# Kernel optimization log

Hardware: AMD Instinct MI355X
Metric: run time of the kernel (lower is better)

## Reference

```python
import jax, jax.numpy as jnp
import numpy as np

NUM_CLASSES = 10
THRESHOLD = 2e-4
ENT_COEF = 2e-4
COS_EPS = 1e-8
LOG_EPS = 1e-12


def setup_inputs() -> dict:
    key = jax.random.key(0)
    k1, k2, k3 = jax.random.split(key, 3)
    B, C, H, W = 256, 256, 8, 8
    M, F = 2000, C * H * W
    z = jax.random.normal(k1, (B, C, H, W), dtype=jnp.float32)
    labels = jax.random.randint(k2, (B,), 0, NUM_CLASSES)
    # kaiming-uniform-like init for the memory table
    bound = float(np.sqrt(6.0 / F))
    memory = jax.random.uniform(k3, (M, F), dtype=jnp.float32, minval=-bound, maxval=bound)
    return {"z": z, "labels": labels, "memory": memory}


def _shrink_l1norm(w):
    # hardshrink (strict |x| > lambda) then L1 renormalize along memories
    w = jnp.where(jnp.abs(w) > THRESHOLD, w, jnp.zeros_like(w))
    return w / jnp.sum(jnp.abs(w), axis=1, keepdims=True)


def _entropy_loss(w):
    return ENT_COEF * jnp.sum(-w * jnp.log(w + LOG_EPS))


def reference(z, labels, memory):
    B, C, H, W = z.shape
    M, F = memory.shape
    zf = z.reshape(B, F)
    # cosine similarity without materializing (B, M, F): dot / max(||z||*||m||, eps)
    nz = jnp.linalg.norm(zf, axis=1)              # (B,)
    nm = jnp.linalg.norm(memory, axis=1)          # (M,)
    logit = (zf @ memory.T) / jnp.maximum(nz[:, None] * nm[None, :], COS_EPS)  # (B, M)
    mem_weight = jax.nn.softmax(logit, axis=1)
    # per-class masks: memory slots are partitioned contiguously per class
    mem_per_class = M // NUM_CLASSES
    cls_of_mem = jnp.arange(M) // mem_per_class   # (M,)
    m1 = (cls_of_mem[None, :] == labels[:, None]).astype(mem_weight.dtype)  # target mask
    m2 = 1.0 - m1
    w_t = _shrink_l1norm(mem_weight * m1)
    w_nt = _shrink_l1norm(mem_weight * m2)
    z_hat_target = (w_t @ memory).reshape(B, C, H, W)
    z_hat_non_target = (w_nt @ memory).reshape(B, C, H, W)
    return (z_hat_target, z_hat_non_target, _entropy_loss(w_t), _entropy_loss(w_nt))
```

## Files before the change

### kernel.cpp

```cpp
#include <hip/hip_runtime.h>
#include <math.h>

#define BATCH 256
#define FDIM 16384
#define MSLOTS 2000
#define MPAD 2048
#define NCLS 10
#define MPC 200
#define NFB2 128

static constexpr float THRESH = 2e-4f;
static constexpr float ENTC   = 2e-4f;
static constexpr float CEPS   = 1e-8f;
static constexpr float LEPS   = 1e-12f;

using bf16x8 = __attribute__((ext_vector_type(8))) short;
using f32x4  = __attribute__((ext_vector_type(4))) float;
using us8    = __attribute__((ext_vector_type(8))) unsigned short;
using f4v    = __attribute__((ext_vector_type(4))) float;
using u4v    = __attribute__((ext_vector_type(4))) unsigned int;

__device__ __forceinline__ unsigned short f2bf(float f) {
  unsigned u = __float_as_uint(f);
  unsigned r = u + 0x7fffu + ((u >> 16) & 1u);
  return (unsigned short)(r >> 16);
}

__device__ __forceinline__ void gload_lds16(const unsigned short* g, unsigned short* l) {
  __builtin_amdgcn_global_load_lds(
      (const __attribute__((address_space(1))) void*)g,
      (__attribute__((address_space(3))) void*)l, 16, 0, 0);
}

__device__ __forceinline__ float waveReduceSum(float v) {
#pragma unroll
  for (int o = 32; o > 0; o >>= 1) v += __shfl_xor(v, o);
  return v;
}
__device__ __forceinline__ float waveReduceMax(float v) {
#pragma unroll
  for (int o = 32; o > 0; o >>= 1) v = fmaxf(v, __shfl_xor(v, o));
  return v;
}


__global__ __launch_bounds__(256) void convert_all_kernel(
    const float* __restrict__ z, const float* __restrict__ mem,
    unsigned short* __restrict__ zb, unsigned short* __restrict__ mb,
    unsigned short* __restrict__ mt, float* __restrict__ npart) {
  __shared__ unsigned int P[64 * 66];
  __shared__ float rsum[64 * 33];
  const int tid = threadIdx.x;
  const int f0 = blockIdx.x * 128;
  const int yt = blockIdx.y;
  const bool isMem = (yt < MPAD / 64);
  const int r0 = isMem ? yt * 64 : (yt - MPAD / 64) * 64;
  const float* src = isMem ? mem : z;
  unsigned short* dst = isMem ? mb : zb;

  const int q = tid & 31;
  const int mb8 = tid >> 5;
  const int fq = f0 + q * 4;

#pragma unroll
  for (int it = 0; it < 8; ++it) {
    const int m = mb8 + it * 8;
    const int gr = r0 + m;
    const bool valid = !isMem || gr < MSLOTS;
    f4v v = (f4v)0.f;
    if (valid)
      v = __builtin_nontemporal_load(
          reinterpret_cast<const f4v*>(&src[(size_t)gr * FDIM + fq]));
    rsum[m * 33 + q] = fmaf(v[0], v[0], fmaf(v[1], v[1], fmaf(v[2], v[2], v[3] * v[3])));
    unsigned lo = ((unsigned)f2bf(v[1]) << 16) | f2bf(v[0]);
    unsigned hi = ((unsigned)f2bf(v[3]) << 16) | f2bf(v[2]);
    *reinterpret_cast<uint2*>(&dst[(size_t)gr * FDIM + fq]) = make_uint2(lo, hi);
    if (isMem) {
      const int x = (m >> 1) & 15;
      *reinterpret_cast<uint2*>(&P[m * 66 + 2 * (q ^ x)]) = make_uint2(lo, hi);
    }
  }
  __syncthreads();

  if (isMem) {
    const int h = tid & 7;
    const int j0 = tid >> 3;
#pragma unroll
    for (int half = 0; half < 2; ++half) {
      const int j = j0 + half * 32;
      unsigned p[8];
#pragma unroll
      for (int s = 0; s < 8; ++s) {
        const int m = h * 8 + s;
        const int col = j ^ (((m >> 1) & 15) << 1);
        p[s] = P[m * 66 + col];
      }
      u4v lo, hi;
#pragma unroll
      for (int t = 0; t < 4; ++t) {
        const unsigned p0 = p[2 * t], p1 = p[2 * t + 1];
        lo[t] = (p1 << 16) | (p0 & 0xFFFFu);
        hi[t] = (p1 & 0xFFFF0000u) | (p0 >> 16);
      }
      const size_t base = (size_t)(f0 + 2 * j) * MPAD + r0 + h * 8;
      *reinterpret_cast<u4v*>(&mt[base])        = lo;
      *reinterpret_cast<u4v*>(&mt[base + MPAD]) = hi;
    }
  }
  if (tid < 64) {
    float s = 0.f;
#pragma unroll
    for (int c = 0; c < 32; ++c) s += rsum[tid * 33 + c];
    const int row = isMem ? (r0 + tid) : (MPAD + r0 + tid);
    npart[(size_t)row * NFB2 + blockIdx.x] = s;
  }
}

__global__ __launch_bounds__(64) void normfin_kernel(const float* __restrict__ npart,
                                                     float* __restrict__ nm,
                                                     float* __restrict__ nz) {
  const int row = blockIdx.x;
  const int lane = threadIdx.x;
  const float* p = npart + (size_t)row * NFB2;
  float s = p[lane] + p[lane + 64];
  s = waveReduceSum(s);
  if (lane == 0) {
    float v = sqrtf(s);
    if (row < MPAD) nm[row] = v;
    else            nz[row - MPAD] = v;
  }
}

#define G1_BM 128
#define G1_BN 64
#define G1_BK 64
#define SPLITK 8
#define KCHUNK (FDIM / SPLITK)

__global__ __launch_bounds__(256, 2) void gemm1_mfma(const unsigned short* __restrict__ zb,
                                                     const unsigned short* __restrict__ mb,
                                                     float* __restrict__ part) {
  __shared__ unsigned short As[G1_BM * G1_BK];
  __shared__ unsigned short Bs[G1_BN * G1_BK];
  const int tid = threadIdx.x;
  const int lane = tid & 63, wid = tid >> 6;
  const int bn0 = blockIdx.x * G1_BN;
  const int bm0 = blockIdx.y * G1_BM;
  const int kbase = blockIdx.z * KCHUNK;
  const int wr = wid >> 1, wc = wid & 1;
  const int l8 = lane >> 3, l7 = lane & 7;
  const int r16 = lane & 15, klane = lane >> 4;

  f32x4 acc[4][2] = {};

  for (int kt = 0; kt < KCHUNK; kt += G1_BK) {
    const int kg = kbase + kt;
#pragma unroll
    for (int it = 0; it < 4; ++it) {
      int c = wid + it * 4;
      int r = c * 8 + l8;
      int src = (l7 ^ (r & 7)) << 3;
      gload_lds16(&zb[(size_t)(bm0 + r) * FDIM + kg + src], &As[c * 512]);
    }
#pragma unroll
    for (int it = 0; it < 2; ++it) {
      int c = wid + it * 4;
      int r = c * 8 + l8;
      int src = (l7 ^ (r & 7)) << 3;
      gload_lds16(&mb[(size_t)(bn0 + r) * FDIM + kg + src], &Bs[c * 512]);
    }
    __syncthreads();
#pragma unroll
    for (int s = 0; s < 2; ++s) {
      bf16x8 a[4], bb[2];
#pragma unroll
      for (int i = 0; i < 4; ++i) {
        int r = wr * 64 + i * 16 + r16;
        int p = (s * 4 + klane) ^ (r & 7);
        a[i] = *reinterpret_cast<const bf16x8*>(&As[r * 64 + p * 8]);
      }
#pragma unroll
      for (int j = 0; j < 2; ++j) {
        int r = wc * 32 + j * 16 + r16;
        int p = (s * 4 + klane) ^ (r & 7);
        bb[j] = *reinterpret_cast<const bf16x8*>(&Bs[r * 64 + p * 8]);
      }
#pragma unroll
      for (int i = 0; i < 4; ++i)
#pragma unroll
        for (int j = 0; j < 2; ++j)
          acc[i][j] = __builtin_amdgcn_mfma_f32_16x16x32_bf16(a[i], bb[j], acc[i][j], 0, 0, 0);
    }
    __syncthreads();
  }
  const int rgrp = lane >> 4;
  float* pbase = part + (size_t)blockIdx.z * BATCH * MPAD;
#pragma unroll
  for (int i = 0; i < 4; ++i)
#pragma unroll
    for (int j = 0; j < 2; ++j)
#pragma unroll
      for (int rg = 0; rg < 4; ++rg) {
        int row = bm0 + wr * 64 + i * 16 + rgrp * 4 + rg;
        int col = bn0 + wc * 32 + j * 16 + r16;
        pbase[(size_t)row * MPAD + col] = acc[i][j][rg];
      }
}

__global__ __launch_bounds__(256) void softmax2_kernel(const float* __restrict__ part,
                                                       const float* __restrict__ nzv,
                                                       const float* __restrict__ nmv,
                                                       const int* __restrict__ labels,
                                                       unsigned short* __restrict__ wt,
                                                       unsigned short* __restrict__ wn,
                                                       float* __restrict__ ent) {
  const int b = blockIdx.x, tid = threadIdx.x;
  __shared__ float sh[MSLOTS];
  __shared__ float red[4], red2[4];
  const float nzb = nzv[b];
  float mx = -3.4e38f;
  for (int m = tid; m < MSLOTS; m += 256) {
    float s = 0.f;
#pragma unroll
    for (int sp = 0; sp < SPLITK; ++sp)
      s += part[((size_t)sp * BATCH + b) * MPAD + m];
    float v = s / fmaxf(nzb * nmv[m], CEPS);
    sh[m] = v; mx = fmaxf(mx, v);
  }
  mx = waveReduceMax(mx);
  if ((tid & 63) == 0) red[tid >> 6] = mx;
  __syncthreads();
  mx = fmaxf(fmaxf(red[0], red[1]), fmaxf(red[2], red[3]));
  __syncthreads();

  float s = 0.f;
  for (int m = tid; m < MSLOTS; m += 256) {
    float e = expf(sh[m] - mx); sh[m] = e; s += e;
  }
  s = waveReduceSum(s);
  if ((tid & 63) == 0) red[tid >> 6] = s;
  __syncthreads();
  s = red[0] + red[1] + red[2] + red[3];
  __syncthreads();

  const float inv = 1.f / s;
  const int c = labels[b];
  const int t0 = c * MPC, t1 = t0 + MPC;
  float st = 0.f, sn = 0.f;
  for (int m = tid; m < MSLOTS; m += 256) {
    float w = sh[m] * inv;
    float k = (w > THRESH) ? w : 0.f;
    sh[m] = k;
    bool tgt = (m >= t0) && (m < t1);
    st += tgt ? k : 0.f;
    sn += tgt ? 0.f : k;
  }
  st = waveReduceSum(st); sn = waveReduceSum(sn);
  if ((tid & 63) == 0) { red[tid >> 6] = st; red2[tid >> 6] = sn; }
  __syncthreads();
  st = red[0] + red[1] + red[2] + red[3];
  sn = red2[0] + red2[1] + red2[2] + red2[3];
  __syncthreads();

  const float rt = 1.f / st, rn = 1.f / sn;
  float et = 0.f, en = 0.f;
  unsigned short* wtr = wt + (size_t)b * MPAD;
  unsigned short* wnr = wn + (size_t)b * MPAD;
  for (int m = tid; m < MPAD; m += 256) {
    float a = 0.f, cn = 0.f;
    if (m < MSLOTS) {
      float k = sh[m];
      bool tgt = (m >= t0) && (m < t1);
      a  = tgt ? k * rt : 0.f;
      cn = tgt ? 0.f : k * rn;
      et -= a  * logf(a  + LEPS);
      en -= cn * logf(cn + LEPS);
    }
    wtr[m] = f2bf(a);
    wnr[m] = f2bf(cn);
  }
  et = waveReduceSum(et); en = waveReduceSum(en);
  if ((tid & 63) == 0) { red[tid >> 6] = et; red2[tid >> 6] = en; }
  __syncthreads();
  if (tid == 0) {
    ent[b]         = red[0] + red[1] + red[2] + red[3];
    ent[BATCH + b] = red2[0] + red2[1] + red2[2] + red2[3];
  }
}

#define G2_BM 128
#define G2_BN 128
#define G2_BK 64

__global__ __launch_bounds__(512, 2) void gemm23_mfma(const unsigned short* __restrict__ wt,
                                                      const unsigned short* __restrict__ wn,
                                                      const unsigned short* __restrict__ mt,
                                                      float* __restrict__ out) {
  __shared__ unsigned short At[G2_BM * G2_BK];
  __shared__ unsigned short An[G2_BM * G2_BK];
  __shared__ unsigned short Bs[G2_BN * G2_BK];
  const int tid = threadIdx.x, lane = tid & 63, wid = tid >> 6;
  const int bn0 = blockIdx.x * G2_BN;
  const int bm0 = blockIdx.y * G2_BM;
  const int wr = wid >> 2, wc = wid & 3;
  const int l8 = lane >> 3, l7 = lane & 7;
  const int r16 = lane & 15, klane = lane >> 4;

  f32x4 acct[4][2] = {}, accn[4][2] = {};

  for (int k0 = 0; k0 < MPAD; k0 += G2_BK) {
#pragma unroll
    for (int it = 0; it < 2; ++it) {
      int c = wid + it * 8;
      int r = c * 8 + l8;
      int src = (l7 ^ (r & 7)) << 3;
      gload_lds16(&wt[(size_t)(bm0 + r) * MPAD + k0 + src], &At[c * 512]);
      gload_lds16(&wn[(size_t)(bm0 + r) * MPAD + k0 + src], &An[c * 512]);
      gload_lds16(&mt[(size_t)(bn0 + r) * MPAD + k0 + src], &Bs[c * 512]);
    }
    __syncthreads();
#pragma unroll
    for (int s = 0; s < 2; ++s) {
      bf16x8 at[4], an[4], bb[2];
#pragma unroll
      for (int i = 0; i < 4; ++i) {
        int r = wr * 64 + i * 16 + r16;
        int p = (s * 4 + klane) ^ (r & 7);
        at[i] = *reinterpret_cast<const bf16x8*>(&At[r * 64 + p * 8]);
        an[i] = *reinterpret_cast<const bf16x8*>(&An[r * 64 + p * 8]);
      }
#pragma unroll
      for (int j = 0; j < 2; ++j) {
        int r = wc * 32 + j * 16 + r16;
        int p = (s * 4 + klane) ^ (r & 7);
        bb[j] = *reinterpret_cast<const bf16x8*>(&Bs[r * 64 + p * 8]);
      }
#pragma unroll
      for (int i = 0; i < 4; ++i)
#pragma unroll
        for (int j = 0; j < 2; ++j) {
          acct[i][j] = __builtin_amdgcn_mfma_f32_16x16x32_bf16(at[i], bb[j], acct[i][j], 0, 0, 0);
          accn[i][j] = __builtin_amdgcn_mfma_f32_16x16x32_bf16(an[i], bb[j], accn[i][j], 0, 0, 0);
        }
    }
    __syncthreads();
  }
  float* outn = out + (size_t)BATCH * FDIM;
  const int rgrp = lane >> 4;
#pragma unroll
  for (int i = 0; i < 4; ++i)
#pragma unroll
    for (int j = 0; j < 2; ++j)
#pragma unroll
      for (int rg = 0; rg < 4; ++rg) {
        size_t off = (size_t)(bm0 + wr * 64 + i * 16 + rgrp * 4 + rg) * FDIM
                   + bn0 + wc * 32 + j * 16 + r16;
        out[off]  = acct[i][j][rg];
        outn[off] = accn[i][j][rg];
      }
}

__global__ __launch_bounds__(256) void entreduce_kernel(const float* __restrict__ ent,
                                                        float* __restrict__ out) {
  const int tid = threadIdx.x;
  float v = ent[tid];
  float u = ent[BATCH + tid];
  v = waveReduceSum(v); u = waveReduceSum(u);
  __shared__ float r1[4], r2[4];
  if ((tid & 63) == 0) { r1[tid >> 6] = v; r2[tid >> 6] = u; }
  __syncthreads();
  if (tid == 0) {
    out[(size_t)2 * BATCH * FDIM]     = ENTC * (r1[0] + r1[1] + r1[2] + r1[3]);
    out[(size_t)2 * BATCH * FDIM + 1] = ENTC * (r2[0] + r2[1] + r2[2] + r2[3]);
  }
}

#define NM_OFF    0
#define NZ_OFF    2048
#define LOGIT_OFF 4096
#define WT_OFF    (LOGIT_OFF + 512000)
#define WNT_OFF   (WT_OFF + 512000)
#define ENT_OFF   (WNT_OFF + 512000)

__global__ __launch_bounds__(256) void rownorm_kernel(const float* __restrict__ x,
                                                      float* __restrict__ out, int cols) {
  const int r = blockIdx.x;
  const float4* xr = reinterpret_cast<const float4*>(x) + (size_t)r * (cols >> 2);
  const int n4 = cols >> 2;
  float s = 0.f;
  for (int i = threadIdx.x; i < n4; i += 256) {
    float4 v = xr[i];
    s = fmaf(v.x, v.x, s); s = fmaf(v.y, v.y, s);
    s = fmaf(v.z, v.z, s); s = fmaf(v.w, v.w, s);
  }
  s = waveReduceSum(s);
  __shared__ float red[4];
  if ((threadIdx.x & 63) == 0) red[threadIdx.x >> 6] = s;
  __syncthreads();
  if (threadIdx.x == 0) out[r] = sqrtf(red[0] + red[1] + red[2] + red[3]);
}

#define O1_BM 64
#define O1_BN 32
#define O1_BK 64
__global__ __launch_bounds__(256) void gemm1_kernel(const float* __restrict__ z,
                                                    const float* __restrict__ mem,
                                                    const float* __restrict__ nzv,
                                                    const float* __restrict__ nmv,
                                                    float* __restrict__ logit) {
  __shared__ float As[O1_BK][O1_BM];
  __shared__ float Bs[O1_BK][O1_BN];
  const int tid = threadIdx.x;
  const int bm0 = blockIdx.y * O1_BM;
  const int bn0 = blockIdx.x * O1_BN;
  const int tm = tid >> 4, tn = tid & 15;
  float acc[4][2] = {};
  for (int k0 = 0; k0 < FDIM; k0 += O1_BK) {
#pragma unroll
    for (int it = 0; it < 4; ++it) {
      int i = tid + it * 256;
      int row = i >> 4, c4 = i & 15;
      float4 v = *reinterpret_cast<const float4*>(&z[(size_t)(bm0 + row) * FDIM + k0 + c4 * 4]);
      As[c4 * 4 + 0][row] = v.x; As[c4 * 4 + 1][row] = v.y;
      As[c4 * 4 + 2][row] = v.z; As[c4 * 4 + 3][row] = v.w;
    }
#pragma unroll
    for (int it = 0; it < 2; ++it) {
      int i = tid + it * 256;
      int row = i >> 4, c4 = i & 15;
      int gm = bn0 + row;
      float4 v = make_float4(0.f, 0.f, 0.f, 0.f);
      if (gm < MSLOTS)
        v = *reinterpret_cast<const float4*>(&mem[(size_t)gm * FDIM + k0 + c4 * 4]);
      Bs[c4 * 4 + 0][row] = v.x; Bs[c4 * 4 + 1][row] = v.y;
      Bs[c4 * 4 + 2][row] = v.z; Bs[c4 * 4 + 3][row] = v.w;
    }
    __syncthreads();
#pragma unroll
    for (int kk = 0; kk < O1_BK; ++kk) {
      const float* ap = &As[kk][tm * 4];
      const float* bp = &Bs[kk][tn * 2];
      float a0 = ap[0], a1 = ap[1], a2 = ap[2], a3 = ap[3];
      float b0 = bp[0], b1 = bp[1];
      acc[0][0] = fmaf(a0, b0, acc[0][0]); acc[0][1] = fmaf(a0, b1, acc[0][1]);
      acc[1][0] = fmaf(a1, b0, acc[1][0]); acc[1][1] = fmaf(a1, b1, acc[1][1]);
      acc[2][0] = fmaf(a2, b0, acc[2][0]); acc[2][1] = fmaf(a2, b1, acc[2][1]);
      acc[3][0] = fmaf(a3, b0, acc[3][0]); acc[3][1] = fmaf(a3, b1, acc[3][1]);
    }
    __syncthreads();
  }
  float nzr[4];
#pragma unroll
  for (int i = 0; i < 4; ++i) nzr[i] = nzv[bm0 + tm * 4 + i];
#pragma unroll
  for (int j = 0; j < 2; ++j) {
    int col = bn0 + tn * 2 + j;
    if (col < MSLOTS) {
      float nmr = nmv[col];
#pragma unroll
      for (int i = 0; i < 4; ++i)
        logit[(size_t)(bm0 + tm * 4 + i) * MSLOTS + col] = acc[i][j] / fmaxf(nzr[i] * nmr, CEPS);
    }
  }
}

__global__ __launch_bounds__(256) void softmax_kernel(const float* __restrict__ logit,
                                                      const int* __restrict__ labels,
                                                      float* __restrict__ wt,
                                                      float* __restrict__ wnt,
                                                      float* __restrict__ ent) {
  const int b = blockIdx.x;
  const int tid = threadIdx.x;
  __shared__ float sh[MSLOTS];
  __shared__ float red[4], red2[4];
  const float* lrow = logit + (size_t)b * MSLOTS;
  float mx = -3.4e38f;
  for (int m = tid; m < MSLOTS; m += 256) {
    float v = lrow[m]; sh[m] = v; mx = fmaxf(mx, v);
  }
  mx = waveReduceMax(mx);
  if ((tid & 63) == 0) red[tid >> 6] = mx;
  __syncthreads();
  mx = fmaxf(fmaxf(red[0], red[1]), fmaxf(red[2], red[3]));
  __syncthreads();
  float s = 0.f;
  for (int m = tid; m < MSLOTS; m += 256) {
    float e = expf(sh[m] - mx); sh[m] = e; s += e;
  }
  s = waveReduceSum(s);
  if ((tid & 63) == 0) red[tid >> 6] = s;
  __syncthreads();
  s = red[0] + red[1] + red[2] + red[3];
  __syncthreads();
  const float inv = 1.f / s;
  const int c = labels[b];
  const int t0 = c * MPC, t1 = t0 + MPC;
  float st = 0.f, sn = 0.f;
  for (int m = tid; m < MSLOTS; m += 256) {
    float w = sh[m] * inv;
    float k = (w > THRESH) ? w : 0.f;
    sh[m] = k;
    bool tgt = (m >= t0) && (m < t1);
    st += tgt ? k : 0.f;
    sn += tgt ? 0.f : k;
  }
  st = waveReduceSum(st); sn = waveReduceSum(sn);
  if ((tid & 63) == 0) { red[tid >> 6] = st; red2[tid >> 6] = sn; }
  __syncthreads();
  st = red[0] + red[1] + red[2] + red[3];
  sn = red2[0] + red2[1] + red2[2] + red2[3];
  __syncthreads();
  const float rt = 1.f / st, rn = 1.f / sn;
  float et = 0.f, en = 0.f;
  float* wtr = wt + (size_t)b * MSLOTS;
  float* wnr = wnt + (size_t)b * MSLOTS;
  for (int m = tid; m < MSLOTS; m += 256) {
    float k = sh[m];
    bool tgt = (m >= t0) && (m < t1);
    float a  = tgt ? k * rt : 0.f;
    float cn = tgt ? 0.f : k * rn;
    wtr[m] = a;
    wnr[m] = cn;
    et -= a  * logf(a  + LEPS);
    en -= cn * logf(cn + LEPS);
  }
  et = waveReduceSum(et); en = waveReduceSum(en);
  if ((tid & 63) == 0) { red[tid >> 6] = et; red2[tid >> 6] = en; }
  __syncthreads();
  if (tid == 0) {
    ent[b]         = red[0] + red[1] + red[2] + red[3];
    ent[BATCH + b] = red2[0] + red2[1] + red2[2] + red2[3];
  }
}

#define O2_BM 64
#define O2_BN 64
#define O2_BK 32
__global__ __launch_bounds__(256) void gemm23_kernel(const float* __restrict__ wt,
                                                     const float* __restrict__ wnt,
                                                     const float* __restrict__ mem,
                                                     float* __restrict__ out) {
  __shared__ float Wts[O2_BK][O2_BM];
  __shared__ float Wns[O2_BK][O2_BM];
  __shared__ float Ms[O2_BK][O2_BN];
  const int tid = threadIdx.x;
  const int bm0 = blockIdx.y * O2_BM;
  const int bn0 = blockIdx.x * O2_BN;
  const int tm = tid >> 4, tn = tid & 15;
  float at[4][4] = {}, an[4][4] = {};
  for (int k0 = 0; k0 < MSLOTS; k0 += O2_BK) {
#pragma unroll
    for (int it = 0; it < 2; ++it) {
      int i = tid + it * 256;
      int row = i >> 3, c4 = i & 7;
      int gk = k0 + c4 * 4;
      float4 vt = make_float4(0.f, 0.f, 0.f, 0.f), vn = vt;
      if (gk < MSLOTS) {
        vt = *reinterpret_cast<const float4*>(&wt [(size_t)(bm0 + row) * MSLOTS + gk]);
        vn = *reinterpret_cast<const float4*>(&wnt[(size_t)(bm0 + row) * MSLOTS + gk]);
      }
      Wts[c4 * 4 + 0][row] = vt.x; Wts[c4 * 4 + 1][row] = vt.y;
      Wts[c4 * 4 + 2][row] = vt.z; Wts[c4 * 4 + 3][row] = vt.w;
      Wns[c4 * 4 + 0][row] = vn.x; Wns[c4 * 4 + 1][row] = vn.y;
      Wns[c4 * 4 + 2][row] = vn.z; Wns[c4 * 4 + 3][row] = vn.w;
    }
#pragma unroll
    for (int it = 0; it < 2; ++it) {
      int i = tid + it * 256;
      int row = i >> 4, c4 = i & 15;
      int gk = k0 + row;
      float4 v = make_float4(0.f, 0.f, 0.f, 0.f);
      if (gk < MSLOTS)
        v = *reinterpret_cast<const float4*>(&mem[(size_t)gk * FDIM + bn0 + c4 * 4]);
      *reinterpret_cast<float4*>(&Ms[row][c4 * 4]) = v;
    }
    __syncthreads();
#pragma unroll
    for (int kk = 0; kk < O2_BK; ++kk) {
      const float* tp = &Wts[kk][tm * 4];
      const float* np = &Wns[kk][tm * 4];
      const float* bp = &Ms[kk][tn * 4];
      float b0 = bp[0], b1 = bp[1], b2 = bp[2], b3 = bp[3];
#pragma unroll
      for (int i = 0; i < 4; ++i) {
        float a = tp[i], cn = np[i];
        at[i][0] = fmaf(a,  b0, at[i][0]); at[i][1] = fmaf(a,  b1, at[i][1]);
        at[i][2] = fmaf(a,  b2, at[i][2]); at[i][3] = fmaf(a,  b3, at[i][3]);
        an[i][0] = fmaf(cn, b0, an[i][0]); an[i][1] = fmaf(cn, b1, an[i][1]);
        an[i][2] = fmaf(cn, b2, an[i][2]); an[i][3] = fmaf(cn, b3, an[i][3]);
      }
    }
    __syncthreads();
  }
  float* outt = out;
  float* outn = out + (size_t)BATCH * FDIM;
#pragma unroll
  for (int i = 0; i < 4; ++i) {
    size_t off = (size_t)(bm0 + tm * 4 + i) * FDIM + bn0 + tn * 4;
    *reinterpret_cast<float4*>(&outt[off]) = make_float4(at[i][0], at[i][1], at[i][2], at[i][3]);
    *reinterpret_cast<float4*>(&outn[off]) = make_float4(an[i][0], an[i][1], an[i][2], an[i][3]);
  }
}

extern "C" void kernel_launch(void* const* d_in, const int* in_sizes, int n_in,
                              void* d_out, int out_size, void* d_ws, size_t ws_size,
                              hipStream_t stream) {
  const float* z      = (const float*)d_in[0];
  const int*   labels = (const int*)d_in[1];
  const float* mem    = (const float*)d_in[2];
  float* out = (float*)d_out;
  char*  wsb = (char*)d_ws;

  constexpr size_t NM_B   = 0;
  constexpr size_t NZ_B   = 8192;
  constexpr size_t ZB_B   = 16384;
  constexpr size_t MB_B   = ZB_B + (size_t)BATCH * FDIM * 2;
  constexpr size_t MT_B   = MB_B + (size_t)MPAD * FDIM * 2;
  constexpr size_t WTB_B  = MT_B + (size_t)FDIM * MPAD * 2;
  constexpr size_t WNB_B  = WTB_B + (size_t)BATCH * MPAD * 2;
  constexpr size_t NP_B   = WNB_B + (size_t)BATCH * MPAD * 2;
  constexpr size_t PART_B = NP_B + (size_t)(MPAD + BATCH) * NFB2 * 4;
  constexpr size_t ENT_B  = PART_B + (size_t)SPLITK * BATCH * MPAD * 4;
  constexpr size_t NEED   = ENT_B + 2048;

  if (ws_size >= NEED) {
    float* nm = (float*)(wsb + NM_B);
    float* nz = (float*)(wsb + NZ_B);
    unsigned short* zb = (unsigned short*)(wsb + ZB_B);
    unsigned short* mb = (unsigned short*)(wsb + MB_B);
    unsigned short* mt = (unsigned short*)(wsb + MT_B);
    unsigned short* wt = (unsigned short*)(wsb + WTB_B);
    unsigned short* wn = (unsigned short*)(wsb + WNB_B);
    float* npart = (float*)(wsb + NP_B);
    float* part  = (float*)(wsb + PART_B);
    float* ent   = (float*)(wsb + ENT_B);

    convert_all_kernel<<<dim3(FDIM / 128, (MPAD + BATCH) / 64), 256, 0, stream>>>(
        z, mem, zb, mb, mt, npart);
    normfin_kernel<<<MPAD + BATCH, 64, 0, stream>>>(npart, nm, nz);
    gemm1_mfma<<<dim3(MPAD / G1_BN, BATCH / G1_BM, SPLITK), 256, 0, stream>>>(zb, mb, part);
    softmax2_kernel<<<BATCH, 256, 0, stream>>>(part, nz, nm, labels, wt, wn, ent);
    gemm23_mfma<<<dim3(FDIM / G2_BN, BATCH / G2_BM), 512, 0, stream>>>(wt, wn, mt, out);
    entreduce_kernel<<<1, 256, 0, stream>>>(ent, out);
  } else {
    float* ws    = (float*)d_ws;
    float* nm    = ws + NM_OFF;
    float* nzv   = ws + NZ_OFF;
    float* logit = ws + LOGIT_OFF;
    float* wt    = ws + WT_OFF;
    float* wnt   = ws + WNT_OFF;
    float* ent   = ws + ENT_OFF;

    rownorm_kernel<<<MSLOTS, 256, 0, stream>>>(mem, nm, FDIM);
    rownorm_kernel<<<BATCH, 256, 0, stream>>>(z, nzv, FDIM);
    gemm1_kernel<<<dim3((MSLOTS + O1_BN - 1) / O1_BN, BATCH / O1_BM), 256, 0, stream>>>(
        z, mem, nzv, nm, logit);
    softmax_kernel<<<BATCH, 256, 0, stream>>>(logit, labels, wt, wnt, ent);
    gemm23_kernel<<<dim3(FDIM / O2_BN, BATCH / O2_BM), 256, 0, stream>>>(wt, wnt, mem, out);
    entreduce_kernel<<<1, 256, 0, stream>>>(ent, out);
  }
}
```

Baseline: 148.2 us.

## Drop transposed memory copy; transpose bf16 memory tiles in LDS inside gemm23

The convert kernel no longer writes a transposed bf16 copy of the memory table, which saves a 64 MB global write and its LDS transpose. The second GEMM now reads the row-major bf16 memory directly into a padded LDS tile with plain vector loads. It then builds the B fragments with eight strided 32-bit LDS reads and a 16-bit extract per element. This removes global traffic but adds scalar LDS reads and ALU work to the GEMM inner loop, and replaces the async global-to-LDS loads for B with register-staged loads.

```diff
diff --git a/kernel.cpp b/kernel.cpp
--- a/kernel.cpp
+++ b/kernel.cpp
@@ -18,7 +18,6 @@
 using f32x4  = __attribute__((ext_vector_type(4))) float;
 using us8    = __attribute__((ext_vector_type(8))) unsigned short;
 using f4v    = __attribute__((ext_vector_type(4))) float;
-using u4v    = __attribute__((ext_vector_type(4))) unsigned int;
 
 __device__ __forceinline__ unsigned short f2bf(float f) {
   unsigned u = __float_as_uint(f);
@@ -47,8 +46,7 @@
 __global__ __launch_bounds__(256) void convert_all_kernel(
     const float* __restrict__ z, const float* __restrict__ mem,
     unsigned short* __restrict__ zb, unsigned short* __restrict__ mb,
-    unsigned short* __restrict__ mt, float* __restrict__ npart) {
-  __shared__ unsigned int P[64 * 66];
+    float* __restrict__ npart) {
   __shared__ float rsum[64 * 33];
   const int tid = threadIdx.x;
   const int f0 = blockIdx.x * 128;
@@ -75,38 +73,8 @@
     unsigned lo = ((unsigned)f2bf(v[1]) << 16) | f2bf(v[0]);
     unsigned hi = ((unsigned)f2bf(v[3]) << 16) | f2bf(v[2]);
     *reinterpret_cast<uint2*>(&dst[(size_t)gr * FDIM + fq]) = make_uint2(lo, hi);
-    if (isMem) {
-      const int x = (m >> 1) & 15;
-      *reinterpret_cast<uint2*>(&P[m * 66 + 2 * (q ^ x)]) = make_uint2(lo, hi);
-    }
-  }
-  __syncthreads();
-
-  if (isMem) {
-    const int h = tid & 7;
-    const int j0 = tid >> 3;
-#pragma unroll
-    for (int half = 0; half < 2; ++half) {
-      const int j = j0 + half * 32;
-      unsigned p[8];
-#pragma unroll
-      for (int s = 0; s < 8; ++s) {
-        const int m = h * 8 + s;
-        const int col = j ^ (((m >> 1) & 15) << 1);
-        p[s] = P[m * 66 + col];
-      }
-      u4v lo, hi;
-#pragma unroll
-      for (int t = 0; t < 4; ++t) {
-        const unsigned p0 = p[2 * t], p1 = p[2 * t + 1];
-        lo[t] = (p1 << 16) | (p0 & 0xFFFFu);
-        hi[t] = (p1 & 0xFFFF0000u) | (p0 >> 16);
-      }
-      const size_t base = (size_t)(f0 + 2 * j) * MPAD + r0 + h * 8;
-      *reinterpret_cast<u4v*>(&mt[base])        = lo;
-      *reinterpret_cast<u4v*>(&mt[base + MPAD]) = hi;
-    }
-  }
+  }
+  __syncthreads();
   if (tid < 64) {
     float s = 0.f;
 #pragma unroll
@@ -294,17 +262,19 @@
 
 __global__ __launch_bounds__(512, 2) void gemm23_mfma(const unsigned short* __restrict__ wt,
                                                       const unsigned short* __restrict__ wn,
-                                                      const unsigned short* __restrict__ mt,
+                                                      const unsigned short* __restrict__ mb,
                                                       float* __restrict__ out) {
   __shared__ unsigned short At[G2_BM * G2_BK];
   __shared__ unsigned short An[G2_BM * G2_BK];
-  __shared__ unsigned short Bs[G2_BN * G2_BK];
+  __shared__ unsigned int   Pb[G2_BK * 66];
   const int tid = threadIdx.x, lane = tid & 63, wid = tid >> 6;
   const int bn0 = blockIdx.x * G2_BN;
   const int bm0 = blockIdx.y * G2_BM;
   const int wr = wid >> 2, wc = wid & 3;
   const int l8 = lane >> 3, l7 = lane & 7;
   const int r16 = lane & 15, klane = lane >> 4;
+  const int fpb = wc * 16 + (r16 >> 1);
+  const int hsh = (r16 & 1) ? 16 : 0;
 
   f32x4 acct[4][2] = {}, accn[4][2] = {};
 
@@ -316,12 +286,20 @@
       int src = (l7 ^ (r & 7)) << 3;
       gload_lds16(&wt[(size_t)(bm0 + r) * MPAD + k0 + src], &At[c * 512]);
       gload_lds16(&wn[(size_t)(bm0 + r) * MPAD + k0 + src], &An[c * 512]);
-      gload_lds16(&mt[(size_t)(bn0 + r) * MPAD + k0 + src], &Bs[c * 512]);
+    }
+#pragma unroll
+    for (int it = 0; it < 2; ++it) {
+      const int t = tid + it * 512;
+      const int r = t & 63, c8 = t >> 6;
+      const uint4 v = *reinterpret_cast<const uint4*>(
+          &mb[(size_t)(k0 + r) * FDIM + bn0 + c8 * 8]);
+      *reinterpret_cast<uint2*>(&Pb[r * 66 + 4 * c8])     = make_uint2(v.x, v.y);
+      *reinterpret_cast<uint2*>(&Pb[r * 66 + 4 * c8 + 2]) = make_uint2(v.z, v.w);
     }
     __syncthreads();
 #pragma unroll
     for (int s = 0; s < 2; ++s) {
-      bf16x8 at[4], an[4], bb[2];
+      bf16x8 at[4], an[4];
 #pragma unroll
       for (int i = 0; i < 4; ++i) {
         int r = wr * 64 + i * 16 + r16;
@@ -331,17 +309,20 @@
       }
 #pragma unroll
       for (int j = 0; j < 2; ++j) {
-        int r = wc * 32 + j * 16 + r16;
-        int p = (s * 4 + klane) ^ (r & 7);
-        bb[j] = *reinterpret_cast<const bf16x8*>(&Bs[r * 64 + p * 8]);
-      }
-#pragma unroll
-      for (int i = 0; i < 4; ++i)
-#pragma unroll
-        for (int j = 0; j < 2; ++j) {
-          acct[i][j] = __builtin_amdgcn_mfma_f32_16x16x32_bf16(at[i], bb[j], acct[i][j], 0, 0, 0);
-          accn[i][j] = __builtin_amdgcn_mfma_f32_16x16x32_bf16(an[i], bb[j], accn[i][j], 0, 0, 0);
+        const int rowb = (s * 32 + klane * 8) * 66 + fpb + j * 8;
+        us8 bv;
+#pragma unroll
+        for (int e = 0; e < 8; ++e) {
+          unsigned pp = Pb[rowb + e * 66];
+          bv[e] = (unsigned short)(pp >> hsh);
         }
+        const bf16x8 bb = *reinterpret_cast<const bf16x8*>(&bv);
+#pragma unroll
+        for (int i = 0; i < 4; ++i) {
+          acct[i][j] = __builtin_amdgcn_mfma_f32_16x16x32_bf16(at[i], bb, acct[i][j], 0, 0, 0);
+          accn[i][j] = __builtin_amdgcn_mfma_f32_16x16x32_bf16(an[i], bb, accn[i][j], 0, 0, 0);
+        }
+      }
     }
     __syncthreads();
   }
@@ -615,8 +596,7 @@
   constexpr size_t NZ_B   = 8192;
   constexpr size_t ZB_B   = 16384;
   constexpr size_t MB_B   = ZB_B + (size_t)BATCH * FDIM * 2;
-  constexpr size_t MT_B   = MB_B + (size_t)MPAD * FDIM * 2;
-  constexpr size_t WTB_B  = MT_B + (size_t)FDIM * MPAD * 2;
+  constexpr size_t WTB_B  = MB_B + (size_t)MPAD * FDIM * 2;
   constexpr size_t WNB_B  = WTB_B + (size_t)BATCH * MPAD * 2;
   constexpr size_t NP_B   = WNB_B + (size_t)BATCH * MPAD * 2;
   constexpr size_t PART_B = NP_B + (size_t)(MPAD + BATCH) * NFB2 * 4;
@@ -628,7 +608,6 @@
     float* nz = (float*)(wsb + NZ_B);
     unsigned short* zb = (unsigned short*)(wsb + ZB_B);
     unsigned short* mb = (unsigned short*)(wsb + MB_B);
-    unsigned short* mt = (unsigned short*)(wsb + MT_B);
     unsigned short* wt = (unsigned short*)(wsb + WTB_B);
     unsigned short* wn = (unsigned short*)(wsb + WNB_B);
     float* npart = (float*)(wsb + NP_B);
@@ -636,11 +615,11 @@
     float* ent   = (float*)(wsb + ENT_B);
 
     convert_all_kernel<<<dim3(FDIM / 128, (MPAD + BATCH) / 64), 256, 0, stream>>>(
-        z, mem, zb, mb, mt, npart);
+        z, mem, zb, mb, npart);
     normfin_kernel<<<MPAD + BATCH, 64, 0, stream>>>(npart, nm, nz);
     gemm1_mfma<<<dim3(MPAD / G1_BN, BATCH / G1_BM, SPLITK), 256, 0, stream>>>(zb, mb, part);
     softmax2_kernel<<<BATCH, 256, 0, stream>>>(part, nz, nm, labels, wt, wn, ent);
-    gemm23_mfma<<<dim3(FDIM / G2_BN, BATCH / G2_BM), 512, 0, stream>>>(wt, wn, mt, out);
+    gemm23_mfma<<<dim3(FDIM / G2_BN, BATCH / G2_BM), 512, 0, stream>>>(wt, wn, mb, out);
     entreduce_kernel<<<1, 256, 0, stream>>>(ent, out);
   } else {
     float* ws    = (float*)d_ws;
```

Result: no change. 148.2 us (+0.0%).
